# Optimization experiments

Measured on AMD Instinct MI355X. Metric: run time of the kernel, lower is better.

The kernel has to match this reference:

```python
import jax, jax.numpy as jnp
from jax import lax
import numpy as np

S, B, D, H, F, K = 1024, 8, 512, 8, 2048, 31
HD = D // H
EPS = 1e-5


def _ln(x, g, b):
    m = jnp.mean(x, axis=-1, keepdims=True)
    v = jnp.mean((x - m) ** 2, axis=-1, keepdims=True)
    return (x - m) * lax.rsqrt(v + EPS) * g + b


def _swish(x):
    return x * jax.nn.sigmoid(x)


def setup_inputs() -> dict:
    key = jax.random.key(0)
    ks = iter(jax.random.split(key, 64))

    def rn(shape, scale=0.02):
        return jax.random.normal(next(ks), shape, dtype=jnp.float32) * scale

    inp = {
        'src': jax.random.normal(next(ks), (S, B, D), dtype=jnp.float32),
        'pos_emb': jax.random.normal(next(ks), (1, 2 * S - 1, D), dtype=jnp.float32),
        # macaron FFN
        'ffm_w1': rn((F, D)), 'ffm_b1': jnp.zeros((F,), jnp.float32),
        'ffm_w2': rn((D, F)), 'ffm_b2': jnp.zeros((D,), jnp.float32),
        # rel-pos MHA
        'in_w': rn((3 * D, D)), 'in_b': jnp.zeros((3 * D,), jnp.float32),
        'out_w': rn((D, D)), 'out_b': jnp.zeros((D,), jnp.float32),
        'pos_w': rn((D, D)),
        'bias_u': rn((H, HD), 0.1), 'bias_v': rn((H, HD), 0.1),
        # conv module
        'pw1_w': rn((2 * D, D)), 'pw1_b': jnp.zeros((2 * D,), jnp.float32),
        'dw_w': rn((D, 1, K)), 'dw_b': jnp.zeros((D,), jnp.float32),
        'cnorm_g': jnp.ones((D,), jnp.float32), 'cnorm_b': jnp.zeros((D,), jnp.float32),
        'pw2_w': rn((D, D)), 'pw2_b': jnp.zeros((D,), jnp.float32),
        # final FFN
        'ff_w1': rn((F, D)), 'ff_b1': jnp.zeros((F,), jnp.float32),
        'ff_w2': rn((D, F)), 'ff_b2': jnp.zeros((D,), jnp.float32),
        # layer norms
        'g_ffm': jnp.ones((D,), jnp.float32), 'b_ffm': jnp.zeros((D,), jnp.float32),
        'g_mha': jnp.ones((D,), jnp.float32), 'b_mha': jnp.zeros((D,), jnp.float32),
        'g_conv': jnp.ones((D,), jnp.float32), 'b_conv': jnp.zeros((D,), jnp.float32),
        'g_ff': jnp.ones((D,), jnp.float32), 'b_ff': jnp.zeros((D,), jnp.float32),
        'g_fin': jnp.ones((D,), jnp.float32), 'b_fin': jnp.zeros((D,), jnp.float32),
    }
    return inp


def _ffn(x, w1, b1, w2, b2):
    return _swish(x @ w1.T + b1) @ w2.T + b2


def _attn(x, pos_emb, in_w, in_b, out_w, out_b, pos_w, bias_u, bias_v):
    # x: (S, B, D)
    qkv = x @ in_w.T + in_b  # (S, B, 3D)
    q, k, v = jnp.split(qkv, 3, axis=-1)
    q = q.reshape(S, B, H, HD).transpose(1, 2, 0, 3)  # (B, H, S, HD)
    k = k.reshape(S, B, H, HD).transpose(1, 2, 0, 3)
    v = v.reshape(S, B, H, HD).transpose(1, 2, 0, 3)
    # positional projection: (2S-1, D) -> (H, HD, 2S-1)
    p = (pos_emb[0] @ pos_w.T).reshape(2 * S - 1, H, HD).transpose(1, 2, 0)
    ac = jnp.einsum('bhsd,bhtd->bhst', q + bias_u[None, :, None, :], k)
    bd = jnp.einsum('bhsd,hdn->bhsn', q + bias_v[None, :, None, :], p)
    # rel_shift: out[b,h,i,j] = bd[b,h,i, (S-1) - i + j]
    idx = (S - 1) - jnp.arange(S)[:, None] + jnp.arange(S)[None, :]  # (S, S)
    bd = jnp.take_along_axis(bd, idx[None, None], axis=-1)  # (B, H, S, S)
    w = jax.nn.softmax((ac + bd) * (HD ** -0.5), axis=-1)
    o = jnp.einsum('bhst,bhtd->bhsd', w, v)
    o = o.transpose(2, 0, 1, 3).reshape(S, B, D)
    return o @ out_w.T + out_b


def _conv_module(x, pw1_w, pw1_b, dw_w, dw_b, cnorm_g, cnorm_b, pw2_w, pw2_b):
    # x: (S, B, D) -> (B, 2D, S)
    y = jnp.einsum('sbd,ed->bes', x, pw1_w) + pw1_b[None, :, None]
    a, g = jnp.split(y, 2, axis=1)
    y = a * jax.nn.sigmoid(g)  # GLU over channels, (B, D, S)
    pad = (K - 1) // 2
    y = lax.conv_general_dilated(y, dw_w, (1,), [(pad, pad)],
                                 dimension_numbers=('NCH', 'OIH', 'NCH'),
                                 feature_group_count=D) + dw_b[None, :, None]
    y = _ln(y.transpose(0, 2, 1), cnorm_g, cnorm_b)  # (B, S, D)
    y = _swish(y)
    y = y @ pw2_w.T + pw2_b  # pointwise conv2 == per-position linear
    return y.transpose(1, 0, 2)  # (S, B, D)


def reference(src, pos_emb, ffm_w1, ffm_b1, ffm_w2, ffm_b2, in_w, in_b, out_w,
              out_b, pos_w, bias_u, bias_v, pw1_w, pw1_b, dw_w, dw_b, cnorm_g,
              cnorm_b, pw2_w, pw2_b, ff_w1, ff_b1, ff_w2, ff_b2, g_ffm, b_ffm,
              g_mha, b_mha, g_conv, b_conv, g_ff, b_ff, g_fin, b_fin):
    x = src
    x = x + 0.5 * _ffn(_ln(x, g_ffm, b_ffm), ffm_w1, ffm_b1, ffm_w2, ffm_b2)
    x = x + _attn(_ln(x, g_mha, b_mha), pos_emb, in_w, in_b, out_w, out_b,
                  pos_w, bias_u, bias_v)
    x = x + _conv_module(_ln(x, g_conv, b_conv), pw1_w, pw1_b, dw_w, dw_b,
                         cnorm_g, cnorm_b, pw2_w, pw2_b)
    x = x + _ffn(_ln(x, g_ff, b_ff), ff_w1, ff_b1, ff_w2, ff_b2)
    return _ln(x, g_fin, b_fin)
```

## Files before the change

### kernel.cpp

```cpp
#include <hip/hip_runtime.h>

typedef __attribute__((ext_vector_type(8))) short bf16x8;
typedef __attribute__((ext_vector_type(4))) short s16x4;
typedef __attribute__((ext_vector_type(4))) float f32x4;
typedef unsigned int u32;

#define SQ 1024
#define BB 8
#define DM 512
#define NH 8
#define HD 64
#define FF 2048
#define NROWS (SQ*BB)

static __device__ __forceinline__ float b2f(short s) {
  return __uint_as_float(((u32)(unsigned short)s) << 16);
}
static __device__ __forceinline__ short f2b(float f) {
  u32 u = __float_as_uint(f);
  return (short)((u + 0x7FFFu + ((u >> 16) & 1u)) >> 16);
}
static __device__ __forceinline__ short f2bt(float f) {
  return (short)((__float_as_uint(f) + 0x8000u) >> 16);
}
static __device__ __forceinline__ float sigm(float x) { return 1.f / (1.f + __expf(-x)); }

static __device__ __forceinline__ f32x4 mfma16(bf16x8 a, bf16x8 b, f32x4 c) {
  return __builtin_amdgcn_mfma_f32_16x16x32_bf16(a, b, c, 0, 0, 0);
}

static __device__ __forceinline__ void gload16(const void* g, void* l) {
  __builtin_amdgcn_global_load_lds(
      (const __attribute__((address_space(1))) void*)g,
      (__attribute__((address_space(3))) void*)l, 16, 0, 0);
}

static __device__ __forceinline__ int swzp(int r, int byteoff) {
  return (r * 128 + byteoff) ^ ((r & 7) << 4);
}

#define WAIT_LGKM() do { \
    asm volatile("s_waitcnt lgkmcnt(0)" ::: "memory"); \
    __builtin_amdgcn_sched_barrier(0); } while (0)
#define WAIT_VM(n) do { \
    asm volatile("s_waitcnt vmcnt(" #n ")" ::: "memory"); \
    __builtin_amdgcn_sched_barrier(0); } while (0)

struct CvtArgs {
  const float* s[10];
  short* d[10];
  int n4[10];
  int cum[10];
};
__global__ __launch_bounds__(256) void cvt_multi(CvtArgs a) {
  int bid = blockIdx.x;
  int seg = 0;
#pragma unroll
  for (int i = 1; i < 10; ++i) if (bid >= a.cum[i]) seg = i;
  int idx = (bid - a.cum[seg]) * 256 + threadIdx.x;
  if (idx >= a.n4[seg]) return;
  float4 v = ((const float4*)a.s[seg])[idx];
  s16x4 r = { f2b(v.x), f2b(v.y), f2b(v.z), f2b(v.w) };
  ((s16x4*)a.d[seg])[idx] = r;
}

template<int MODE, int INF32>
__global__ __launch_bounds__(256) void ln_kernel(const void* __restrict__ xin,
                                                 const float* __restrict__ gam,
                                                 const float* __restrict__ bet,
                                                 void* __restrict__ out) {
  int w = threadIdx.x >> 6, lane = threadIdx.x & 63;
  int row = (blockIdx.x << 2) + w;
  float v[8];
  if (INF32) {
    const float* xr = (const float*)xin + (size_t)row * DM + lane * 8;
    float4 a = *(const float4*)xr;
    float4 c = *(const float4*)(xr + 4);
    v[0]=a.x; v[1]=a.y; v[2]=a.z; v[3]=a.w; v[4]=c.x; v[5]=c.y; v[6]=c.z; v[7]=c.w;
  } else {
    bf16x8 x8 = *(const bf16x8*)((const short*)xin + (size_t)row * DM + lane * 8);
#pragma unroll
    for (int e = 0; e < 8; ++e) v[e] = b2f(x8[e]);
  }
  float s = 0.f, q = 0.f;
#pragma unroll
  for (int e = 0; e < 8; ++e) { s += v[e]; q += v[e] * v[e]; }
#pragma unroll
  for (int m = 1; m < 64; m <<= 1) { s += __shfl_xor(s, m); q += __shfl_xor(q, m); }
  float mean = s * (1.f / DM);
  float rstd = rsqrtf(q * (1.f / DM) - mean * mean + 1e-5f);
  int col = lane * 8;
  if (MODE == 1) {
    float* o = (float*)out + (size_t)row * DM + col;
    float y[8];
#pragma unroll
    for (int e = 0; e < 8; ++e) y[e] = (v[e] - mean) * rstd * gam[col + e] + bet[col + e];
    *(float4*)o = make_float4(y[0], y[1], y[2], y[3]);
    *(float4*)(o + 4) = make_float4(y[4], y[5], y[6], y[7]);
  } else {
    bf16x8 r;
#pragma unroll
    for (int e = 0; e < 8; ++e) {
      float y = (v[e] - mean) * rstd * gam[col + e] + bet[col + e];
      r[e] = f2b(y);
    }
    *(bf16x8*)((short*)out + (size_t)row * DM + col) = r;
  }
}

template<int EPI>
__global__ __launch_bounds__(512, 2) void gemm256(const short* __restrict__ A,
                                                  const short* __restrict__ W,
                                                  const float* __restrict__ bias,
                                                  short* __restrict__ out,
                                                  int M, int N, int K) {
  __shared__ __align__(16) short lds[3 * 16384];
  int nb = N >> 8;
  int nwg = gridDim.x, bid = blockIdx.x;
  int bid2 = ((nwg & 7) == 0) ? ((bid & 7) * (nwg >> 3) + (bid >> 3)) : bid;
  int bm = bid2 / nb, bn = bid2 % nb;
  int m0 = bm << 8, n0 = bn << 8;
  int tid = threadIdx.x, w = tid >> 6, lane = tid & 63;
  int wm = w >> 2, wn = w & 3;
  int l15 = lane & 15, l4 = lane >> 4;
  int srow = lane >> 2;
  int slog = (lane & 3) ^ (((lane >> 5) & 1) << 1);
  int scol = slog << 3;

  const short* gsrc = (w < 4) ? (A + (size_t)(m0 + w * 64 + srow) * K + scol)
                              : (W + (size_t)(n0 + (w - 4) * 64 + srow) * K + scol);

  f32x4 acc[8][4];
#pragma unroll
  for (int i = 0; i < 8; ++i)
#pragma unroll
    for (int j = 0; j < 4; ++j) acc[i][j] = (f32x4){0.f, 0.f, 0.f, 0.f};

  auto stage2 = [&](int u, int kt, int q0) {
#pragma unroll
    for (int q = q0; q < q0 + 2; ++q)
      gload16(gsrc + (size_t)(q * 16) * K + kt,
              (char*)lds + u * 32768 + (w * 4 + q) * 1024);
  };
  auto rdA = [&](int u, int mf) -> bf16x8 {
    int ps = l4 ^ (((l15 >> 3) & 1) << 1);
    return *(const bf16x8*)((char*)lds + u * 32768 + (wm * 8 + mf) * 1024 + l15 * 64 + ps * 16);
  };
  auto rdB = [&](int u, int nf) -> bf16x8 {
    int ps = l4 ^ (((l15 >> 3) & 1) << 1);
    return *(const bf16x8*)((char*)lds + u * 32768 + 16384 + (wn * 4 + nf) * 1024 + l15 * 64 + ps * 16);
  };

  int nt = K >> 5;
  stage2(0, 0, 0); stage2(0, 0, 2);
  stage2(1, 32, 0); stage2(1, 32, 2);
  WAIT_VM(4);
  __builtin_amdgcn_s_barrier();

  int u = 0;
  for (int t = 0; t < nt; ++t) {
    int kt2 = (t + 2) << 5;
    int us = u + 2; if (us >= 3) us -= 3;
    bool st = (t + 2) < nt;
    bf16x8 afrag[4], bfrag[4];
#pragma unroll
    for (int nf = 0; nf < 4; ++nf) bfrag[nf] = rdB(u, nf);
#pragma unroll
    for (int mf = 0; mf < 4; ++mf) afrag[mf] = rdA(u, mf);
    if (st) stage2(us, kt2, 0);
    __builtin_amdgcn_s_barrier();
    WAIT_LGKM();
    __builtin_amdgcn_s_setprio(1);
#pragma unroll
    for (int mf = 0; mf < 4; ++mf)
#pragma unroll
      for (int nf = 0; nf < 4; ++nf)
        acc[mf][nf] = mfma16(afrag[mf], bfrag[nf], acc[mf][nf]);
    __builtin_amdgcn_s_setprio(0);
    __builtin_amdgcn_s_barrier();
#pragma unroll
    for (int mf = 0; mf < 4; ++mf) afrag[mf] = rdA(u, mf + 4);
    if (st) stage2(us, kt2, 2);
    __builtin_amdgcn_s_barrier();
    WAIT_LGKM();
    __builtin_amdgcn_s_setprio(1);
#pragma unroll
    for (int mf = 0; mf < 4; ++mf)
#pragma unroll
      for (int nf = 0; nf < 4; ++nf)
        acc[mf + 4][nf] = mfma16(afrag[mf], bfrag[nf], acc[mf + 4][nf]);
    __builtin_amdgcn_s_setprio(0);
    if (t < nt - 1) {
      if (st) { WAIT_VM(4); } else { WAIT_VM(0); }
    }
    __builtin_amdgcn_s_barrier();
    ++u; if (u >= 3) u -= 3;
  }

#pragma unroll
  for (int nf = 0; nf < 4; ++nf) {
    int col = n0 + wn * 64 + nf * 16 + l15;
    float bv = bias[col];
#pragma unroll
    for (int mf = 0; mf < 8; ++mf) {
#pragma unroll
      for (int r4 = 0; r4 < 4; ++r4) {
        int row = m0 + wm * 128 + mf * 16 + l4 * 4 + r4;
        float v = acc[mf][nf][r4] + bv;
        if (EPI == 1) v = v * sigm(v);
        out[(size_t)row * N + col] = f2b(v);
      }
    }
  }
}

template<int EPI, int RESF32>
__global__ __launch_bounds__(256) void gemm_bt(const short* __restrict__ A,
                                               const short* __restrict__ W,
                                               const float* __restrict__ bias,
                                               const void* __restrict__ res,
                                               float alpha, short* __restrict__ out,
                                               int M, int N, int K) {
  __shared__ __align__(16) short ldsA[2 * 128 * 32];
  __shared__ __align__(16) short ldsB[2 * 128 * 32];
  int nb = N >> 7;
  int nwg = gridDim.x, bid = blockIdx.x;
  int bid2 = ((nwg & 7) == 0) ? ((bid & 7) * (nwg >> 3) + (bid >> 3)) : bid;
  int bm = bid2 / nb, bn = bid2 % nb;
  int m0 = bm << 7, n0 = bn << 7;
  int tid = threadIdx.x, w = tid >> 6, lane = tid & 63;
  int wm = w >> 1, wn = w & 1;
  f32x4 acc[4][4];
#pragma unroll
  for (int i = 0; i < 4; ++i)
#pragma unroll
    for (int j = 0; j < 4; ++j) acc[i][j] = (f32x4){0.f, 0.f, 0.f, 0.f};

  auto stage = [&](int bufsel, int kt) {
#pragma unroll
    for (int q = 0; q < 2; ++q) {
      int c = (q * 4 + w) * 64 + lane;
      int r = c >> 2, cc = c & 3;
      gload16(A + (size_t)(m0 + r) * K + kt + cc * 8,
              (char*)ldsA + bufsel * 8192 + (q * 4 + w) * 1024);
      gload16(W + (size_t)(n0 + r) * K + kt + cc * 8,
              (char*)ldsB + bufsel * 8192 + (q * 4 + w) * 1024);
    }
  };

  stage(0, 0);
  asm volatile("s_waitcnt vmcnt(0)" ::: "memory");
  __syncthreads();
  int cur = 0;
  for (int kt = 0; kt < K; kt += 32) {
    if (kt + 32 < K) stage(cur ^ 1, kt + 32);
    int rr = lane & 15, kk = (lane >> 4) << 3;
    bf16x8 af[4], bfr[4];
#pragma unroll
    for (int mt = 0; mt < 4; ++mt)
      af[mt] = *(const bf16x8*)(ldsA + cur * 4096 + (wm * 64 + mt * 16 + rr) * 32 + kk);
#pragma unroll
    for (int nt = 0; nt < 4; ++nt)
      bfr[nt] = *(const bf16x8*)(ldsB + cur * 4096 + (wn * 64 + nt * 16 + rr) * 32 + kk);
#pragma unroll
    for (int mt = 0; mt < 4; ++mt)
#pragma unroll
      for (int nt = 0; nt < 4; ++nt)
        acc[mt][nt] = mfma16(af[mt], bfr[nt], acc[mt][nt]);
    asm volatile("s_waitcnt vmcnt(0)" ::: "memory");
    __syncthreads();
    cur ^= 1;
  }

#pragma unroll
  for (int mt = 0; mt < 4; ++mt) {
#pragma unroll
    for (int nt = 0; nt < 4; ++nt) {
      int col = n0 + wn * 64 + nt * 16 + (lane & 15);
      float bv = (EPI == 3) ? 0.f : bias[col];
#pragma unroll
      for (int r4 = 0; r4 < 4; ++r4) {
        int row = m0 + wm * 64 + mt * 16 + (lane >> 4) * 4 + r4;
        size_t idx = (size_t)row * N + col;
        float v = acc[mt][nt][r4] + bv;
        if (EPI == 3) {
          out[idx] = f2b(v);
        } else {
          float rv = RESF32 ? ((const float*)res)[idx] : b2f(((const short*)res)[idx]);
          out[idx] = f2b(rv + alpha * v);
        }
      }
    }
  }
}

__global__ __launch_bounds__(256) void prep_kernel(const short* __restrict__ qkv,
                                                   short* __restrict__ VTp) {
  __shared__ short ldsv[64 * 66];
  int tid = threadIdx.x;
  int st = blockIdx.x & 15, bh = blockIdx.x >> 4;
  int b = bh >> 3, h = bh & 7;
  int s0 = st << 6;
#pragma unroll
  for (int pass = 0; pass < 2; ++pass) {
    int r = pass * 32 + (tid >> 3), c = tid & 7;
    int s = s0 + r;
    bf16x8 v8 = *(const bf16x8*)(qkv + (size_t)(s * BB + b) * 1536 + 1024 + h * 64 + c * 8);
    *(bf16x8*)(ldsv + r * 66 + c * 8) = v8;
  }
  __syncthreads();
#pragma unroll
  for (int pass = 0; pass < 2; ++pass) {
    int d = pass * 32 + (tid >> 3), sc = tid & 7;
    bf16x8 o;
#pragma unroll
    for (int u = 0; u < 8; ++u) o[u] = ldsv[(sc * 8 + u) * 66 + d];
    *(bf16x8*)(VTp + ((size_t)bh * 64 + d) * SQ + s0 + sc * 8) = o;
  }
}

__global__ __launch_bounds__(512, 4) void attn_kernel(const short* __restrict__ qkv,
                                                      const short* __restrict__ VTp,
                                                      const short* __restrict__ posb,
                                                      const float* __restrict__ bias_u,
                                                      const float* __restrict__ bias_v,
                                                      short* __restrict__ obuf) {
  __shared__ __align__(16) char smem[78848];
  char* lds_k   = smem;
  char* lds_vt  = smem + 16384;
  char* lds_pos = smem + 24576;
  char* lds_ew  = smem + 57344;

  int tid = threadIdx.x, w = tid >> 6, lane = tid & 63;
  int l15 = lane & 15, l4 = lane >> 4;
  int it = blockIdx.x >> 6, bh = blockIdx.x & 63;
  int b = bh >> 3, h = bh & 7;
  int i0 = it << 7;
  char* ewb = lds_ew + w * 2688;

  const size_t hoffB = (size_t)bh * SQ * 128;

  const float SC2 = 0.125f * 1.44269504f;
  int fr = i0 + w * 16 + l15;
  const short* qrow = qkv + (size_t)(fr * BB + b) * 1536 + h * 64;
  bf16x8 qu_f[2], qv_f[2];
#pragma unroll
  for (int ks = 0; ks < 2; ++ks) {
    bf16x8 qraw = *(const bf16x8*)(qrow + ks * 32 + l4 * 8);
#pragma unroll
    for (int e = 0; e < 8; ++e) {
      float qf = b2f(qraw[e]);
      int d = h * 64 + ks * 32 + l4 * 8 + e;
      qu_f[ks][e] = f2b((qf + bias_u[d]) * SC2);
      qv_f[ks][e] = f2b((qf + bias_v[d]) * SC2);
    }
  }

  float m_run = -1e30f, l_run = 0.f;
  f32x4 o_acc[4];
#pragma unroll
  for (int dt = 0; dt < 4; ++dt) o_acc[dt] = (f32x4){0.f, 0.f, 0.f, 0.f};

  int prbase = 112 - 16 * w;
  int lnq = lane >> 3, lnr = lane & 7;
  int r8 = w * 8 + lnq;
  int byt = (lnr * 16) ^ ((r8 & 7) << 4);
  int nbase = 896 - i0;

  auto stageK = [&](int t1) {
    int j = (t1 << 6) + r8;
    gload16((const char*)qkv + (size_t)(j * BB + b) * 3072 + 1024 + h * 128 + byt,
            lds_k + (t1 & 1) * 8192 + w * 1024);
  };
  auto stageVT = [&](int t1) {
    gload16((const char*)VTp + hoffB + (size_t)r8 * 2048 + (size_t)(t1 << 7) + byt,
            lds_vt + w * 1024);
  };
  auto stagePosSeg = [&](int gbase, int pseg) {
    gload16((const char*)posb + (size_t)(gbase + r8) * 1024 + h * 128 + byt,
            lds_pos + pseg * 8192 + w * 1024);
  };

  stagePosSeg(nbase, 0);
  stagePosSeg(nbase + 64, 1);
  stagePosSeg(nbase + 128, 2);
  stageK(0);
  WAIT_VM(0);

  for (int t = 0; t < 16; ++t) {
    int cur = t & 1;
    __builtin_amdgcn_s_barrier();
    stageVT(t);

    f32x4 acs[4];
    __builtin_amdgcn_s_setprio(1);
#pragma unroll
    for (int kt = 0; kt < 4; ++kt) {
      f32x4 z = (f32x4){0.f, 0.f, 0.f, 0.f};
      bf16x8 kb0 = *(const bf16x8*)(lds_k + cur * 8192 + swzp(kt * 16 + l15, l4 * 16));
      bf16x8 kb1 = *(const bf16x8*)(lds_k + cur * 8192 + swzp(kt * 16 + l15, 64 + l4 * 16));
      z = mfma16(kb0, qu_f[0], z);
      z = mfma16(kb1, qu_f[1], z);
      acs[kt] = z;
    }
    __builtin_amdgcn_s_setprio(0);
#pragma unroll
    for (int pt = 0; pt < 5; ++pt) {
      f32x4 z = (f32x4){0.f, 0.f, 0.f, 0.f};
      int pr = prbase + pt * 16 + l15;
      char* pbase = lds_pos + (((t + (pr >> 6)) & 3) * 8192);
      bf16x8 pb0 = *(const bf16x8*)(pbase + swzp(pr & 63, l4 * 16));
      bf16x8 pb1 = *(const bf16x8*)(pbase + swzp(pr & 63, 64 + l4 * 16));
      __builtin_amdgcn_s_setprio(1);
      z = mfma16(pb0, qv_f[0], z);
      z = mfma16(pb1, qv_f[1], z);
      __builtin_amdgcn_s_setprio(0);
      s16x4 ek;
#pragma unroll
      for (int r = 0; r < 4; ++r) ek[r] = f2bt(z[r]);
      *(s16x4*)(ewb + (l15 * 84 + pt * 16 + l4 * 4) * 2) = ek;
    }

    bool pf = (t + 1) < 16;
    if (pf) {
      stageK(t + 1);
      stagePosSeg(nbase + (t << 6) + 192, (t + 3) & 3);
    }

    WAIT_LGKM();

    float sv[4][4];
    float mt = -1e30f;
#pragma unroll
    for (int kt = 0; kt < 4; ++kt) {
#pragma unroll
      for (int r = 0; r < 4; ++r) {
        int n = 15 - l15 + kt * 16 + l4 * 4 + r;
        float ev = b2f(*(const short*)(ewb + (l15 * 84 + n) * 2));
        float sc = acs[kt][r] + ev;
        sv[kt][r] = sc;
        mt = fmaxf(mt, sc);
      }
    }
    if (!__all(mt <= m_run + 11.5415604f)) {
      float mr = fmaxf(mt, __shfl_xor(mt, 16));
      mr = fmaxf(mr, __shfl_xor(mr, 32));
      float mn = fmaxf(m_run, mr);
      float fac = exp2f(m_run - mn);
      m_run = mn;
      l_run *= fac;
      float fb[4];
#pragma unroll
      for (int r4 = 0; r4 < 4; ++r4) fb[r4] = __shfl(fac, (l4 << 2) + r4);
#pragma unroll
      for (int dt = 0; dt < 4; ++dt)
#pragma unroll
        for (int r4 = 0; r4 < 4; ++r4) o_acc[dt][r4] *= fb[r4];
    }
    float ls = 0.f;
#pragma unroll
    for (int kt = 0; kt < 4; ++kt) {
      s16x4 pk;
#pragma unroll
      for (int r = 0; r < 4; ++r) {
        float p = exp2f(sv[kt][r] - m_run);
        ls += p;
        pk[r] = f2bt(p);
      }
      *(s16x4*)(ewb + l15 * 128 + ((kt * 32 + l4 * 8) ^ ((l15 & 7) << 4))) = pk;
    }
    l_run += ls;

    if (pf) { WAIT_VM(2); } else { WAIT_VM(0); }
    WAIT_LGKM();
    __builtin_amdgcn_s_barrier();

    bf16x8 pa[2];
#pragma unroll
    for (int ks = 0; ks < 2; ++ks)
      pa[ks] = *(const bf16x8*)(ewb + swzp(l15, ks * 64 + l4 * 16));
    __builtin_amdgcn_s_setprio(1);
#pragma unroll
    for (int dt = 0; dt < 4; ++dt) {
      bf16x8 vb0 = *(const bf16x8*)(lds_vt + swzp(dt * 16 + l15, l4 * 16));
      bf16x8 vb1 = *(const bf16x8*)(lds_vt + swzp(dt * 16 + l15, 64 + l4 * 16));
      o_acc[dt] = mfma16(pa[0], vb0, o_acc[dt]);
      o_acc[dt] = mfma16(pa[1], vb1, o_acc[dt]);
    }
    __builtin_amdgcn_s_setprio(0);

    WAIT_VM(0);
  }

  float lt = l_run + __shfl_xor(l_run, 16);
  lt += __shfl_xor(lt, 32);
  float lb[4];
#pragma unroll
  for (int r4 = 0; r4 < 4; ++r4) lb[r4] = __shfl(lt, (l4 << 2) + r4);
#pragma unroll
  for (int dt = 0; dt < 4; ++dt) {
#pragma unroll
    for (int r4 = 0; r4 < 4; ++r4) {
      int i = i0 + w * 16 + l4 * 4 + r4;
      int d = dt * 16 + l15;
      float val = o_acc[dt][r4] / lb[r4];
      obuf[(size_t)(i * BB + b) * DM + h * 64 + d] = f2b(val);
    }
  }
}

__global__ __launch_bounds__(256) void glu_dwconv_kernel(const short* __restrict__ pw1,
                                                         const float* __restrict__ dww,
                                                         const float* __restrict__ dwb,
                                                         const float* __restrict__ cg,
                                                         const float* __restrict__ cb,
                                                         short* __restrict__ outbf) {
  __shared__ short glu[38 * 512];
  __shared__ float red[8][4][2];
  int tid = threadIdx.x;
  int b = blockIdx.x & 7;
  int s0 = (blockIdx.x >> 3) << 3;
  for (int idx = tid; idx < 38 * 64; idx += 256) {
    int r = idx >> 6, c8 = idx & 63;
    int s = s0 - 15 + r;
    bf16x8 res;
    if (s >= 0 && s < SQ) {
      const short* row = pw1 + (size_t)(s * BB + b) * 1024;
      bf16x8 a8 = *(const bf16x8*)(row + c8 * 8);
      bf16x8 g8 = *(const bf16x8*)(row + 512 + c8 * 8);
#pragma unroll
      for (int e = 0; e < 8; ++e) res[e] = f2b(b2f(a8[e]) * sigm(b2f(g8[e])));
    } else {
#pragma unroll
      for (int e = 0; e < 8; ++e) res[e] = 0;
    }
    *(bf16x8*)(glu + r * 512 + c8 * 8) = res;
  }
  __syncthreads();

  float a0[8], a1[8];
  {
    float wreg[31];
#pragma unroll
    for (int k = 0; k < 31; ++k) wreg[k] = dww[tid * 31 + k];
    float bb = dwb[tid];
    for (int ri = 0; ri < 8; ++ri) {
      float acc = bb;
#pragma unroll
      for (int k = 0; k < 31; ++k)
        acc += wreg[k] * b2f(glu[(ri + k) * 512 + tid]);
      a0[ri] = acc;
    }
  }
  {
    int d = tid + 256;
    float wreg[31];
#pragma unroll
    for (int k = 0; k < 31; ++k) wreg[k] = dww[d * 31 + k];
    float bb = dwb[d];
    for (int ri = 0; ri < 8; ++ri) {
      float acc = bb;
#pragma unroll
      for (int k = 0; k < 31; ++k)
        acc += wreg[k] * b2f(glu[(ri + k) * 512 + d]);
      a1[ri] = acc;
    }
  }

  int w = tid >> 6, lane = tid & 63;
#pragma unroll
  for (int ri = 0; ri < 8; ++ri) {
    float sp = a0[ri] + a1[ri];
    float qp = a0[ri] * a0[ri] + a1[ri] * a1[ri];
#pragma unroll
    for (int m = 1; m < 64; m <<= 1) { sp += __shfl_xor(sp, m); qp += __shfl_xor(qp, m); }
    if (lane == 0) { red[ri][w][0] = sp; red[ri][w][1] = qp; }
  }
  __syncthreads();
  float g0 = cg[tid], b0 = cb[tid], g1 = cg[tid + 256], b1 = cb[tid + 256];
#pragma unroll
  for (int ri = 0; ri < 8; ++ri) {
    float s = red[ri][0][0] + red[ri][1][0] + red[ri][2][0] + red[ri][3][0];
    float q = red[ri][0][1] + red[ri][1][1] + red[ri][2][1] + red[ri][3][1];
    float mean = s * (1.f / DM);
    float rstd = rsqrtf(q * (1.f / DM) - mean * mean + 1e-5f);
    float y0 = (a0[ri] - mean) * rstd * g0 + b0;
    float y1 = (a1[ri] - mean) * rstd * g1 + b1;
    y0 = y0 * sigm(y0);
    y1 = y1 * sigm(y1);
    size_t base = (size_t)((s0 + ri) * BB + b) * 512;
    outbf[base + tid] = f2b(y0);
    outbf[base + tid + 256] = f2b(y1);
  }
}

extern "C" void kernel_launch(void* const* d_in, const int* in_sizes, int n_in,
                              void* d_out, int out_size, void* d_ws, size_t ws_size,
                              hipStream_t stream) {
  const float* src    = (const float*)d_in[0];
  const float* pose   = (const float*)d_in[1];
  const float* ffm_w1 = (const float*)d_in[2];
  const float* ffm_b1 = (const float*)d_in[3];
  const float* ffm_w2 = (const float*)d_in[4];
  const float* ffm_b2 = (const float*)d_in[5];
  const float* in_w   = (const float*)d_in[6];
  const float* in_b   = (const float*)d_in[7];
  const float* out_w  = (const float*)d_in[8];
  const float* out_b  = (const float*)d_in[9];
  const float* pos_w  = (const float*)d_in[10];
  const float* bias_u = (const float*)d_in[11];
  const float* bias_v = (const float*)d_in[12];
  const float* pw1_w  = (const float*)d_in[13];
  const float* pw1_b  = (const float*)d_in[14];
  const float* dw_w   = (const float*)d_in[15];
  const float* dw_b   = (const float*)d_in[16];
  const float* cng    = (const float*)d_in[17];
  const float* cnb    = (const float*)d_in[18];
  const float* pw2_w  = (const float*)d_in[19];
  const float* pw2_b  = (const float*)d_in[20];
  const float* ff_w1  = (const float*)d_in[21];
  const float* ff_b1  = (const float*)d_in[22];
  const float* ff_w2  = (const float*)d_in[23];
  const float* ff_b2  = (const float*)d_in[24];
  const float* g_ffm  = (const float*)d_in[25];
  const float* b_ffm  = (const float*)d_in[26];
  const float* g_mha  = (const float*)d_in[27];
  const float* b_mha  = (const float*)d_in[28];
  const float* g_conv = (const float*)d_in[29];
  const float* b_conv = (const float*)d_in[30];
  const float* g_ff   = (const float*)d_in[31];
  const float* b_ff   = (const float*)d_in[32];
  const float* g_fin  = (const float*)d_in[33];
  const float* b_fin  = (const float*)d_in[34];

  char* ws = (char*)d_ws;
  size_t off = 0;
  auto alloc = [&](size_t bytes) -> void* {
    void* p = ws + off;
    off += (bytes + 255) & ~(size_t)255;
    return p;
  };
  short* wb_ffm1 = (short*)alloc((size_t)FF * DM * 2);
  short* wb_ffm2 = (short*)alloc((size_t)DM * FF * 2);
  short* wb_in   = (short*)alloc((size_t)3 * DM * DM * 2);
  short* wb_out  = (short*)alloc((size_t)DM * DM * 2);
  short* wb_pos  = (short*)alloc((size_t)DM * DM * 2);
  short* wb_pw1  = (short*)alloc((size_t)2 * DM * DM * 2);
  short* wb_pw2  = (short*)alloc((size_t)DM * DM * 2);
  short* wb_ff1  = (short*)alloc((size_t)FF * DM * 2);
  short* wb_ff2  = (short*)alloc((size_t)DM * FF * 2);
  short* pos_src = (short*)alloc((size_t)2048 * DM * 2);
  short* pos_bf  = (short*)alloc((size_t)2048 * DM * 2);
  short* lnb     = (short*)alloc((size_t)NROWS * DM * 2);
  short* hbig    = (short*)alloc((size_t)NROWS * FF * 2);
  short* qkvb    = (short*)alloc((size_t)NROWS * 3 * DM * 2);
  short* obuf    = (short*)alloc((size_t)NROWS * DM * 2);
  short* x1      = (short*)alloc((size_t)NROWS * DM * 2);
  short* x2      = (short*)alloc((size_t)NROWS * DM * 2);
  short* pw1raw  = hbig;
  short* convy   = obuf;
  short* x3 = x1;
  short* x4 = x2;
  short* VTp = hbig + (size_t)3 * 4194304;

  CvtArgs ca;
  const float* srcs[10] = {ffm_w1, ffm_w2, in_w, out_w, pos_w, pw1_w, pw2_w, ff_w1, ff_w2, pose};
  short* dsts[10] = {wb_ffm1, wb_ffm2, wb_in, wb_out, wb_pos, wb_pw1, wb_pw2, wb_ff1, wb_ff2, pos_src};
  size_t ns[10] = {(size_t)FF*DM, (size_t)DM*FF, (size_t)3*DM*DM, (size_t)DM*DM, (size_t)DM*DM,
                   (size_t)2*DM*DM, (size_t)DM*DM, (size_t)FF*DM, (size_t)DM*FF, (size_t)2047*DM};
  int cum = 0;
  for (int i = 0; i < 10; ++i) {
    ca.s[i] = srcs[i]; ca.d[i] = dsts[i];
    ca.n4[i] = (int)(ns[i] >> 2);
    ca.cum[i] = cum;
    cum += (ca.n4[i] + 255) / 256;
  }
  cvt_multi<<<dim3(cum), dim3(256), 0, stream>>>(ca);

  auto gemmR = [&](int RESF32, const short* A, const short* W, const float* bias,
                   const void* res, float alpha, short* out, int M, int N, int K) {
    dim3 g((M / 128) * (N / 128)), blk(256);
    if (RESF32) gemm_bt<2, 1><<<g, blk, 0, stream>>>(A, W, bias, res, alpha, out, M, N, K);
    else        gemm_bt<2, 0><<<g, blk, 0, stream>>>(A, W, bias, res, alpha, out, M, N, K);
  };
  auto gemm2 = [&](int EPI, const short* A, const short* W, const float* bias,
                   short* out, int M, int N, int K) {
    dim3 g((M / 256) * (N / 256)), blk(512);
    if (EPI == 0) gemm256<0><<<g, blk, 0, stream>>>(A, W, bias, out, M, N, K);
    else          gemm256<1><<<g, blk, 0, stream>>>(A, W, bias, out, M, N, K);
  };

  gemm_bt<3, 0><<<dim3(64), dim3(256), 0, stream>>>(pos_src, wb_pos, nullptr, nullptr, 0.f,
                                                    pos_bf, 2048, DM, DM);

  ln_kernel<0, 1><<<dim3(NROWS / 4), dim3(256), 0, stream>>>(src, g_ffm, b_ffm, lnb);
  gemm2(1, lnb, wb_ffm1, ffm_b1, hbig, NROWS, FF, DM);
  gemmR(1, hbig, wb_ffm2, ffm_b2, src, 0.5f, x1, NROWS, DM, FF);

  ln_kernel<0, 0><<<dim3(NROWS / 4), dim3(256), 0, stream>>>(x1, g_mha, b_mha, lnb);
  gemm2(0, lnb, wb_in, in_b, qkvb, NROWS, 3 * DM, DM);
  prep_kernel<<<dim3(1024), dim3(256), 0, stream>>>(qkvb, VTp);
  attn_kernel<<<dim3(512), dim3(512), 0, stream>>>(qkvb, VTp, pos_bf, bias_u, bias_v, obuf);
  gemmR(0, obuf, wb_out, out_b, x1, 1.f, x2, NROWS, DM, DM);

  ln_kernel<0, 0><<<dim3(NROWS / 4), dim3(256), 0, stream>>>(x2, g_conv, b_conv, lnb);
  gemm2(0, lnb, wb_pw1, pw1_b, pw1raw, NROWS, 2 * DM, DM);
  glu_dwconv_kernel<<<dim3(1024), dim3(256), 0, stream>>>(pw1raw, dw_w, dw_b, cng, cnb, convy);
  gemmR(0, convy, wb_pw2, pw2_b, x2, 1.f, x3, NROWS, DM, DM);

  ln_kernel<0, 0><<<dim3(NROWS / 4), dim3(256), 0, stream>>>(x3, g_ff, b_ff, lnb);
  gemm2(1, lnb, wb_ff1, ff_b1, hbig, NROWS, FF, DM);
  gemmR(0, hbig, wb_ff2, ff_b2, x3, 1.f, x4, NROWS, DM, FF);

  ln_kernel<1, 0><<<dim3(NROWS / 4), dim3(256), 0, stream>>>(x4, g_fin, b_fin, d_out);

  (void)in_sizes; (void)n_in; (void)out_size; (void)ws_size;
}
```

Measured before the change: 375.3 us.

## Rewrite 128-tile GEMM with triple-buffered LDS, swizzled layout and warp-specialized loads

The 128x128 GEMM used for the residual projections now uses a three-stage LDS ring with prefetch two tiles ahead and partial vmcnt waits in place of full drains. Each wave loads a contiguous 64-row slab of A or W. A XOR swizzle on the LDS layout is meant to cut bank conflicts on fragment reads. It also raises MFMA priority and sets launch bounds for 3 blocks per CU, trading more LDS per block for fewer pipeline stalls.

Result: faster. 329.8 us (-12.1%).

```diff
diff --git a/kernel.cpp b/kernel.cpp
--- a/kernel.cpp
+++ b/kernel.cpp
@@ -215,14 +215,13 @@
 }
 
 template<int EPI, int RESF32>
-__global__ __launch_bounds__(256) void gemm_bt(const short* __restrict__ A,
-                                               const short* __restrict__ W,
-                                               const float* __restrict__ bias,
-                                               const void* __restrict__ res,
-                                               float alpha, short* __restrict__ out,
-                                               int M, int N, int K) {
-  __shared__ __align__(16) short ldsA[2 * 128 * 32];
-  __shared__ __align__(16) short ldsB[2 * 128 * 32];
+__global__ __launch_bounds__(256, 3) void gemm128(const short* __restrict__ A,
+                                                  const short* __restrict__ W,
+                                                  const float* __restrict__ bias,
+                                                  const void* __restrict__ res,
+                                                  float alpha, short* __restrict__ out,
+                                                  int M, int N, int K) {
+  __shared__ __align__(16) short lds[3 * 8192];
   int nb = N >> 7;
   int nwg = gridDim.x, bid = blockIdx.x;
   int bid2 = ((nwg & 7) == 0) ? ((bid & 7) * (nwg >> 3) + (bid >> 3)) : bid;
@@ -230,59 +229,78 @@
   int m0 = bm << 7, n0 = bn << 7;
   int tid = threadIdx.x, w = tid >> 6, lane = tid & 63;
   int wm = w >> 1, wn = w & 1;
+  int l15 = lane & 15, l4 = lane >> 4;
+  int srow = lane >> 2;
+  int slog = (lane & 3) ^ (((lane >> 5) & 1) << 1);
+  int scol = slog << 3;
+
+  const short* gsrc = (w < 2) ? (A + (size_t)(m0 + w * 64 + srow) * K + scol)
+                              : (W + (size_t)(n0 + (w - 2) * 64 + srow) * K + scol);
+  int ldsbase = w * 4096;
+
   f32x4 acc[4][4];
 #pragma unroll
   for (int i = 0; i < 4; ++i)
 #pragma unroll
     for (int j = 0; j < 4; ++j) acc[i][j] = (f32x4){0.f, 0.f, 0.f, 0.f};
 
-  auto stage = [&](int bufsel, int kt) {
-#pragma unroll
-    for (int q = 0; q < 2; ++q) {
-      int c = (q * 4 + w) * 64 + lane;
-      int r = c >> 2, cc = c & 3;
-      gload16(A + (size_t)(m0 + r) * K + kt + cc * 8,
-              (char*)ldsA + bufsel * 8192 + (q * 4 + w) * 1024);
-      gload16(W + (size_t)(n0 + r) * K + kt + cc * 8,
-              (char*)ldsB + bufsel * 8192 + (q * 4 + w) * 1024);
-    }
-  };
-
+  auto stage = [&](int u, int kt) {
+#pragma unroll
+    for (int q = 0; q < 4; ++q)
+      gload16(gsrc + (size_t)(q * 16) * K + kt,
+              (char*)lds + u * 16384 + ldsbase + q * 1024);
+  };
+  auto rdA = [&](int u, int mf) -> bf16x8 {
+    int ps = l4 ^ (((l15 >> 3) & 1) << 1);
+    return *(const bf16x8*)((char*)lds + u * 16384 + (wm * 4 + mf) * 1024 + l15 * 64 + ps * 16);
+  };
+  auto rdB = [&](int u, int nf) -> bf16x8 {
+    int ps = l4 ^ (((l15 >> 3) & 1) << 1);
+    return *(const bf16x8*)((char*)lds + u * 16384 + 8192 + (wn * 4 + nf) * 1024 + l15 * 64 + ps * 16);
+  };
+
+  int nt = K >> 5;
   stage(0, 0);
-  asm volatile("s_waitcnt vmcnt(0)" ::: "memory");
-  __syncthreads();
-  int cur = 0;
-  for (int kt = 0; kt < K; kt += 32) {
-    if (kt + 32 < K) stage(cur ^ 1, kt + 32);
-    int rr = lane & 15, kk = (lane >> 4) << 3;
-    bf16x8 af[4], bfr[4];
-#pragma unroll
-    for (int mt = 0; mt < 4; ++mt)
-      af[mt] = *(const bf16x8*)(ldsA + cur * 4096 + (wm * 64 + mt * 16 + rr) * 32 + kk);
-#pragma unroll
-    for (int nt = 0; nt < 4; ++nt)
-      bfr[nt] = *(const bf16x8*)(ldsB + cur * 4096 + (wn * 64 + nt * 16 + rr) * 32 + kk);
-#pragma unroll
-    for (int mt = 0; mt < 4; ++mt)
-#pragma unroll
-      for (int nt = 0; nt < 4; ++nt)
-        acc[mt][nt] = mfma16(af[mt], bfr[nt], acc[mt][nt]);
-    asm volatile("s_waitcnt vmcnt(0)" ::: "memory");
-    __syncthreads();
-    cur ^= 1;
-  }
-
-#pragma unroll
-  for (int mt = 0; mt < 4; ++mt) {
-#pragma unroll
-    for (int nt = 0; nt < 4; ++nt) {
-      int col = n0 + wn * 64 + nt * 16 + (lane & 15);
+  stage(1, 32);
+  WAIT_VM(4);
+  __builtin_amdgcn_s_barrier();
+
+  int u = 0;
+  for (int t = 0; t < nt; ++t) {
+    int us = u + 2; if (us >= 3) us -= 3;
+    bool st = (t + 2) < nt;
+    bf16x8 afrag[4], bfrag[4];
+#pragma unroll
+    for (int mf = 0; mf < 4; ++mf) afrag[mf] = rdA(u, mf);
+#pragma unroll
+    for (int nf = 0; nf < 4; ++nf) bfrag[nf] = rdB(u, nf);
+    if (st) stage(us, (t + 2) << 5);
+    WAIT_LGKM();
+    __builtin_amdgcn_s_setprio(1);
+#pragma unroll
+    for (int mf = 0; mf < 4; ++mf)
+#pragma unroll
+      for (int nf = 0; nf < 4; ++nf)
+        acc[mf][nf] = mfma16(afrag[mf], bfrag[nf], acc[mf][nf]);
+    __builtin_amdgcn_s_setprio(0);
+    if (t < nt - 1) {
+      if (st) { WAIT_VM(4); } else { WAIT_VM(0); }
+    }
+    __builtin_amdgcn_s_barrier();
+    ++u; if (u >= 3) u -= 3;
+  }
+
+#pragma unroll
+  for (int mf = 0; mf < 4; ++mf) {
+#pragma unroll
+    for (int nf = 0; nf < 4; ++nf) {
+      int col = n0 + wn * 64 + nf * 16 + l15;
       float bv = (EPI == 3) ? 0.f : bias[col];
 #pragma unroll
       for (int r4 = 0; r4 < 4; ++r4) {
-        int row = m0 + wm * 64 + mt * 16 + (lane >> 4) * 4 + r4;
+        int row = m0 + wm * 64 + mf * 16 + l4 * 4 + r4;
         size_t idx = (size_t)row * N + col;
-        float v = acc[mt][nt][r4] + bv;
+        float v = acc[mf][nf][r4] + bv;
         if (EPI == 3) {
           out[idx] = f2b(v);
         } else {
@@ -680,8 +698,8 @@
   auto gemmR = [&](int RESF32, const short* A, const short* W, const float* bias,
                    const void* res, float alpha, short* out, int M, int N, int K) {
     dim3 g((M / 128) * (N / 128)), blk(256);
-    if (RESF32) gemm_bt<2, 1><<<g, blk, 0, stream>>>(A, W, bias, res, alpha, out, M, N, K);
-    else        gemm_bt<2, 0><<<g, blk, 0, stream>>>(A, W, bias, res, alpha, out, M, N, K);
+    if (RESF32) gemm128<2, 1><<<g, blk, 0, stream>>>(A, W, bias, res, alpha, out, M, N, K);
+    else        gemm128<2, 0><<<g, blk, 0, stream>>>(A, W, bias, res, alpha, out, M, N, K);
   };
   auto gemm2 = [&](int EPI, const short* A, const short* W, const float* bias,
                    short* out, int M, int N, int K) {
@@ -690,7 +708,7 @@
     else          gemm256<1><<<g, blk, 0, stream>>>(A, W, bias, out, M, N, K);
   };
 
-  gemm_bt<3, 0><<<dim3(64), dim3(256), 0, stream>>>(pos_src, wb_pos, nullptr, nullptr, 0.f,
+  gemm128<3, 0><<<dim3(64), dim3(256), 0, stream>>>(pos_src, wb_pos, nullptr, nullptr, 0.f,
                                                     pos_bf, 2048, DM, DM);
 
   ln_kernel<0, 1><<<dim3(NROWS / 4), dim3(256), 0, stream>>>(src, g_ffm, b_ffm, lnb);
```
